# Performance work log

Hardware: AMD Instinct MI355X
Metric: run time of the kernel (lower is better)

## Reference

```python
import jax, jax.numpy as jnp
import numpy as np

E, C, D, H = 32, 4096, 256, 1024

def setup_inputs() -> dict:
    key = jax.random.key(0)
    kx, k1, k2 = jax.random.split(key, 3)
    x = jax.random.normal(kx, (E, C, D), dtype=jnp.float32)
    w1 = jax.random.normal(k1, (E, D, H), dtype=jnp.float32) * 0.02
    w2 = jax.random.normal(k2, (E, H, D), dtype=jnp.float32) * 0.02
    b1 = jnp.zeros((E, H), dtype=jnp.float32)
    b2 = jnp.zeros((E, D), dtype=jnp.float32)
    bungee = jnp.ones((E,), dtype=jnp.float32)  # bungee_init = 1.0, per-expert
    return {"x": x, "w1": w1, "b1": b1, "w2": w2, "b2": b2, "bungee": bungee}

def reference(x, w1, b1, w2, b2, bungee):
    # per-expert MLP: [E,C,D] @ [E,D,H] -> bias -> exact GELU -> [E,C,H] @ [E,H,D] -> bias -> scale
    h = jnp.einsum('ecd,edh->ech', x, w1) + b1[:, None, :]
    h = jax.nn.gelu(h, approximate=False)
    y = jnp.einsum('ech,ehd->ecd', h, w2) + b2[:, None, :]
    y = y * bungee[:, None, None]
    expert_out_rms = jnp.sqrt(jnp.mean(jnp.square(y)))
    bungee_mean = jnp.mean(bungee)
    bungee_min = jnp.min(bungee)
    bungee_max = jnp.max(bungee)
    return (y, expert_out_rms, bungee_mean, bungee_min, bungee_max)
```

## Files before the change

### kernel.cpp

```cpp
#include <hip/hip_runtime.h>
#include <cmath>

#define NE 32
#define NC 4096
#define ND 256
#define NH 1024
#define BM 64
#define BH 128
#define NSTEP (NH / BH)
#define NWAVE 8
#define THREADS (NWAVE * 64)
#define NWG (NE * NC / BM)
#define TOTY ((size_t)NE * NC * ND)

typedef float  float4v __attribute__((ext_vector_type(4)));
typedef float  f32x4   __attribute__((ext_vector_type(4)));
typedef short  short8v __attribute__((ext_vector_type(8)));
typedef short  short4v __attribute__((ext_vector_type(4)));
typedef __bf16 bf16x8  __attribute__((ext_vector_type(8)));
typedef __bf16 bf16x4  __attribute__((ext_vector_type(4)));

__device__ inline unsigned short f2bf(float f) {
  unsigned int u = __float_as_uint(f);
  u += 0x7fffu + ((u >> 16) & 1u);
  return (unsigned short)(u >> 16);
}

__device__ inline f32x4 mfma16(bf16x8 a, bf16x8 b, f32x4 c) {
  return __builtin_amdgcn_mfma_f32_16x16x32_bf16(a, b, c, 0, 0, 0);
}

__device__ inline float gelu_fast(float v) {
  float u = v * 0.70710678118f;
  float a = fabsf(u);
  float t = __builtin_amdgcn_rcpf(__builtin_fmaf(0.3275911f, a, 1.0f));
  float p = 1.061405429f;
  p = __builtin_fmaf(p, t, -1.453152027f);
  p = __builtin_fmaf(p, t, 1.421413741f);
  p = __builtin_fmaf(p, t, -0.284496736f);
  p = __builtin_fmaf(p, t, 0.254829592f);
  p = p * t;
  float e = __expf(-u * u);
  float erf_a = 1.0f - p * e;
  float erf_u = copysignf(erf_a, u);
  return 0.5f * v * (1.0f + erf_u);
}

__device__ inline float gelu_exact(float v) {
  return 0.5f * v * (1.0f + erff(v * 0.70710678118f));
}

__global__ void transpose_cvt(const float* __restrict__ src, unsigned short* __restrict__ dst,
                              int R, int Cc) {
  __shared__ alignas(16) float tile[32][33];
  int tilesC = Cc >> 5;
  int per_e  = (R >> 5) * tilesC;
  int e  = blockIdx.x / per_e;
  int t  = blockIdx.x % per_e;
  int tr = t / tilesC, tc = t % tilesC;
  const float* s = src + (size_t)e * R * Cc;
  unsigned short* d = dst + (size_t)e * R * Cc;
  int tx = threadIdx.x & 31, ty = threadIdx.x >> 5;
  for (int i = ty; i < 32; i += 8)
    tile[i][tx] = s[(size_t)(tr * 32 + i) * Cc + tc * 32 + tx];
  __syncthreads();
  for (int i = ty; i < 32; i += 8)
    d[(size_t)(tc * 32 + i) * R + tr * 32 + tx] = f2bf(tile[tx][i]);
}

__global__ void zero_scalar(float* p) {
  if (threadIdx.x == 0 && blockIdx.x == 0) *p = 0.0f;
}

__global__ __launch_bounds__(THREADS, 4) void experts_mlp(
    const float* __restrict__ x, const float* __restrict__ b1,
    const float* __restrict__ b2, const float* __restrict__ bungee,
    const unsigned short* __restrict__ w1t, const unsigned short* __restrict__ w2t,
    float* __restrict__ y, float* __restrict__ sumsq) {
  __shared__ alignas(16) unsigned char x_sw[BM * 512];
  __shared__ alignas(16) short h_lds[BM][BH + 8];
  __shared__ float red[NWAVE];

  int bid = blockIdx.x;
  int wg  = (bid & 7) * (NWG / 8) + (bid >> 3);
  int e   = wg >> 6;
  int r0  = (wg & 63) * BM;

  int tid  = threadIdx.x;
  int wid  = tid >> 6;
  int lane = tid & 63;
  int lr   = lane & 15;
  int lg   = lane >> 4;
  int lr7  = lr & 7;

  {
    const float* xb = x + ((size_t)e * NC + r0) * ND;
    #pragma unroll
    for (int j = 0; j < 8; ++j) {
      int f   = j * 512 + tid;
      int row = f >> 6;
      int c16 = f & 63;
      float4v u = *(const float4v*)(xb + (size_t)f * 4);
      bf16x4 s;
      s[0] = (__bf16)u[0]; s[1] = (__bf16)u[1]; s[2] = (__bf16)u[2]; s[3] = (__bf16)u[3];
      int cb = c16 * 8;
      *(bf16x4*)(x_sw + row * 512 + (cb ^ ((row & 7) << 6))) = s;
    }
  }
  __syncthreads();

  f32x4 zero4 = {0.f, 0.f, 0.f, 0.f};
  f32x4 acc2[2][4];
  #pragma unroll
  for (int mf = 0; mf < 2; ++mf)
    #pragma unroll
    for (int nf = 0; nf < 4; ++nf) acc2[mf][nf] = zero4;

  const unsigned short* w1row = w1t + ((size_t)e * NH + wid * 16 + lr) * ND;
  const unsigned short* w2row = w2t + ((size_t)e * ND + wid * 32 + lr) * NH;

  for (int hs = 0; hs < NSTEP; ++hs) {
    bf16x8 a1[8];
    const unsigned short* wr = w1row + (size_t)hs * BH * ND;
    #pragma unroll
    for (int ks = 0; ks < 8; ++ks)
      a1[ks] = __builtin_bit_cast(bf16x8, *(const short8v*)(wr + ks * 32 + lg * 8));

    f32x4 acc1[4];
    #pragma unroll
    for (int nf = 0; nf < 4; ++nf) acc1[nf] = zero4;
    #pragma unroll
    for (int ks = 0; ks < 8; ++ks) {
      int kx = (ks ^ lr7) * 64 + lg * 16;
      #pragma unroll
      for (int nf = 0; nf < 4; ++nf) {
        int row = nf * 16 + lr;
        bf16x8 xv = *(const bf16x8*)(x_sw + row * 512 + kx);
        acc1[nf] = mfma16(a1[ks], xv, acc1[nf]);
      }
    }

    int clocal = wid * 16 + lg * 4;
    const float* b1p = b1 + (size_t)e * NH + hs * BH + clocal;
    float4v bv = *(const float4v*)b1p;
    #pragma unroll
    for (int nf = 0; nf < 4; ++nf) {
      bf16x4 p;
      #pragma unroll
      for (int reg = 0; reg < 4; ++reg)
        p[reg] = (__bf16)gelu_fast(acc1[nf][reg] + bv[reg]);
      *(bf16x4*)&h_lds[nf * 16 + lr][clocal] = p;
    }
    __syncthreads();

    const unsigned short* w2p = w2row + (size_t)hs * BH;
    #pragma unroll
    for (int ks = 0; ks < 4; ++ks) {
      bf16x8 a20 = __builtin_bit_cast(bf16x8, *(const short8v*)(w2p + ks * 32 + lg * 8));
      bf16x8 a21 = __builtin_bit_cast(bf16x8, *(const short8v*)(w2p + (size_t)16 * NH + ks * 32 + lg * 8));
      #pragma unroll
      for (int nf = 0; nf < 4; ++nf) {
        bf16x8 hb = __builtin_bit_cast(bf16x8, *(const short8v*)&h_lds[nf * 16 + lr][ks * 32 + lg * 8]);
        acc2[0][nf] = mfma16(a20, hb, acc2[0][nf]);
        acc2[1][nf] = mfma16(a21, hb, acc2[1][nf]);
      }
    }
    __syncthreads();
  }

  float bg = bungee[e];
  float ss = 0.0f;
  int dbase = wid * 32 + lg * 4;
  #pragma unroll
  for (int mf = 0; mf < 2; ++mf) {
    int dd = dbase + mf * 16;
    float4v b2v = *(const float4v*)(b2 + (size_t)e * ND + dd);
    #pragma unroll
    for (int nf = 0; nf < 4; ++nf) {
      int r = r0 + nf * 16 + lr;
      float4v o;
      #pragma unroll
      for (int reg = 0; reg < 4; ++reg) {
        float v = (acc2[mf][nf][reg] + b2v[reg]) * bg;
        o[reg] = v;
        ss += v * v;
      }
      *(float4v*)(y + ((size_t)e * NC + r) * ND + dd) = o;
    }
  }
  #pragma unroll
  for (int off = 32; off > 0; off >>= 1) ss += __shfl_down(ss, off);
  if (lane == 0) red[wid] = ss;
  __syncthreads();
  if (tid == 0) {
    float t = 0.f;
    #pragma unroll
    for (int i = 0; i < NWAVE; ++i) t += red[i];
    atomicAdd(sumsq, t);
  }
}

#define FBROWS 8
__global__ __launch_bounds__(256) void fb_mlp(
    const float* __restrict__ x, const float* __restrict__ w1, const float* __restrict__ b1,
    const float* __restrict__ w2, const float* __restrict__ b2, const float* __restrict__ bungee,
    float* __restrict__ y, float* __restrict__ sumsq) {
  __shared__ alignas(16) float xs[FBROWS][ND];
  __shared__ alignas(16) float hsh[FBROWS][NH];
  __shared__ float red[4];
  int tid = threadIdx.x;
  int e  = blockIdx.x / (NC / FBROWS);
  int r0 = (blockIdx.x % (NC / FBROWS)) * FBROWS;

  for (int i = tid; i < FBROWS * ND; i += 256)
    ((float*)xs)[i] = x[((size_t)e * NC + r0) * ND + i];
  __syncthreads();

  for (int c = tid; c < NH; c += 256) {
    float acc[FBROWS];
    float bb = b1[(size_t)e * NH + c];
    #pragma unroll
    for (int rr = 0; rr < FBROWS; ++rr) acc[rr] = bb;
    for (int k = 0; k < ND; ++k) {
      float w = w1[((size_t)e * ND + k) * NH + c];
      #pragma unroll
      for (int rr = 0; rr < FBROWS; ++rr) acc[rr] += xs[rr][k] * w;
    }
    #pragma unroll
    for (int rr = 0; rr < FBROWS; ++rr) hsh[rr][c] = gelu_exact(acc[rr]);
  }
  __syncthreads();

  int d = tid;
  float acc[FBROWS];
  float bb = b2[(size_t)e * ND + d];
  #pragma unroll
  for (int rr = 0; rr < FBROWS; ++rr) acc[rr] = bb;
  for (int c = 0; c < NH; ++c) {
    float w = w2[((size_t)e * NH + c) * ND + d];
    #pragma unroll
    for (int rr = 0; rr < FBROWS; ++rr) acc[rr] += hsh[rr][c] * w;
  }
  float bg = bungee[e];
  float ss = 0.f;
  #pragma unroll
  for (int rr = 0; rr < FBROWS; ++rr) {
    float v = acc[rr] * bg;
    y[((size_t)e * NC + r0 + rr) * ND + d] = v;
    ss += v * v;
  }
  #pragma unroll
  for (int off = 32; off > 0; off >>= 1) ss += __shfl_down(ss, off);
  if ((tid & 63) == 0) red[tid >> 6] = ss;
  __syncthreads();
  if (tid == 0) atomicAdd(sumsq, red[0] + red[1] + red[2] + red[3]);
}

__global__ void finalize(const float* __restrict__ bungee, float* __restrict__ out_scalars) {
  if (threadIdx.x == 0 && blockIdx.x == 0) {
    float ss = out_scalars[0];
    out_scalars[0] = sqrtf(ss / (float)TOTY);
    float m = 0.f, mn = bungee[0], mx = bungee[0];
    for (int i = 0; i < NE; ++i) {
      float b = bungee[i];
      m += b; mn = fminf(mn, b); mx = fmaxf(mx, b);
    }
    out_scalars[1] = m / (float)NE;
    out_scalars[2] = mn;
    out_scalars[3] = mx;
  }
}

extern "C" void kernel_launch(void* const* d_in, const int* in_sizes, int n_in,
                              void* d_out, int out_size, void* d_ws, size_t ws_size,
                              hipStream_t stream) {
  (void)in_sizes; (void)n_in; (void)out_size;
  const float* x  = (const float*)d_in[0];
  const float* w1 = (const float*)d_in[1];
  const float* b1 = (const float*)d_in[2];
  const float* w2 = (const float*)d_in[3];
  const float* b2 = (const float*)d_in[4];
  const float* bg = (const float*)d_in[5];
  float* out = (float*)d_out;
  float* rms_slot = out + TOTY;

  const size_t WS_NEEDED = (size_t)NE * ND * NH * 2 * 2;

  zero_scalar<<<1, 1, 0, stream>>>(rms_slot);
  if (ws_size >= WS_NEEDED) {
    unsigned short* w1t = (unsigned short*)d_ws;
    unsigned short* w2t = w1t + (size_t)NE * ND * NH;
    transpose_cvt<<<NE * (ND / 32) * (NH / 32), 256, 0, stream>>>(w1, w1t, ND, NH);
    transpose_cvt<<<NE * (NH / 32) * (ND / 32), 256, 0, stream>>>(w2, w2t, NH, ND);
    experts_mlp<<<NWG, THREADS, 0, stream>>>(x, b1, b2, bg, w1t, w2t, out, rms_slot);
  } else {
    fb_mlp<<<NE * NC / FBROWS, 256, 0, stream>>>(x, w1, b1, w2, b2, bg, out, rms_slot);
  }
  finalize<<<1, 64, 0, stream>>>(bg, rms_slot);
}
```

Measured before the change: 547.2 us.

## Prefetch next-step W1 fragments and hoist W2 loads; fuse prep kernels

Software-pipelines the weight fragment loads in the expert MLP loop. W2 fragments are issued at the top of each step and the next step's W1 fragments are loaded after the first GEMM, so global latency overlaps with MFMA work. The first W1 load moves ahead of the initial barrier. The two transpose kernels and the zeroing kernel are merged into one prep launch to cut launch overhead. The added in-flight fragments raise register pressure, which may reduce occupancy under the 4-waves launch bound.

```diff
diff --git a/kernel.cpp b/kernel.cpp
--- a/kernel.cpp
+++ b/kernel.cpp
@@ -50,13 +50,19 @@
   return 0.5f * v * (1.0f + erff(v * 0.70710678118f));
 }
 
-__global__ void transpose_cvt(const float* __restrict__ src, unsigned short* __restrict__ dst,
-                              int R, int Cc) {
+__global__ void prep(const float* __restrict__ w1, const float* __restrict__ w2,
+                     unsigned short* __restrict__ w1t, unsigned short* __restrict__ w2t,
+                     float* __restrict__ rms_slot) {
+  if (blockIdx.x == 0 && threadIdx.x == 0) *rms_slot = 0.0f;
   __shared__ alignas(16) float tile[32][33];
+  int b = blockIdx.x;
+  const float* src; unsigned short* dst; int R, Cc;
+  if (b < 8192) { src = w1; dst = w1t; R = ND; Cc = NH; }
+  else          { b -= 8192; src = w2; dst = w2t; R = NH; Cc = ND; }
   int tilesC = Cc >> 5;
   int per_e  = (R >> 5) * tilesC;
-  int e  = blockIdx.x / per_e;
-  int t  = blockIdx.x % per_e;
+  int e  = b / per_e;
+  int t  = b % per_e;
   int tr = t / tilesC, tc = t % tilesC;
   const float* s = src + (size_t)e * R * Cc;
   unsigned short* d = dst + (size_t)e * R * Cc;
@@ -107,7 +113,6 @@
       *(bf16x4*)(x_sw + row * 512 + (cb ^ ((row & 7) << 6))) = s;
     }
   }
-  __syncthreads();
 
   f32x4 zero4 = {0.f, 0.f, 0.f, 0.f};
   f32x4 acc2[2][4];
@@ -119,12 +124,21 @@
   const unsigned short* w1row = w1t + ((size_t)e * NH + wid * 16 + lr) * ND;
   const unsigned short* w2row = w2t + ((size_t)e * ND + wid * 32 + lr) * NH;
 
+  bf16x8 a1[8];
+  #pragma unroll
+  for (int ks = 0; ks < 8; ++ks)
+    a1[ks] = __builtin_bit_cast(bf16x8, *(const short8v*)(w1row + ks * 32 + lg * 8));
+
+  __syncthreads();
+
   for (int hs = 0; hs < NSTEP; ++hs) {
-    bf16x8 a1[8];
-    const unsigned short* wr = w1row + (size_t)hs * BH * ND;
-    #pragma unroll
-    for (int ks = 0; ks < 8; ++ks)
-      a1[ks] = __builtin_bit_cast(bf16x8, *(const short8v*)(wr + ks * 32 + lg * 8));
+    const unsigned short* w2p = w2row + (size_t)hs * BH;
+    bf16x8 w2f0[4], w2f1[4];
+    #pragma unroll
+    for (int ks = 0; ks < 4; ++ks) {
+      w2f0[ks] = __builtin_bit_cast(bf16x8, *(const short8v*)(w2p + ks * 32 + lg * 8));
+      w2f1[ks] = __builtin_bit_cast(bf16x8, *(const short8v*)(w2p + (size_t)16 * NH + ks * 32 + lg * 8));
+    }
 
     f32x4 acc1[4];
     #pragma unroll
@@ -140,6 +154,13 @@
       }
     }
 
+    if (hs + 1 < NSTEP) {
+      const unsigned short* wr = w1row + (size_t)(hs + 1) * BH * ND;
+      #pragma unroll
+      for (int ks = 0; ks < 8; ++ks)
+        a1[ks] = __builtin_bit_cast(bf16x8, *(const short8v*)(wr + ks * 32 + lg * 8));
+    }
+
     int clocal = wid * 16 + lg * 4;
     const float* b1p = b1 + (size_t)e * NH + hs * BH + clocal;
     float4v bv = *(const float4v*)b1p;
@@ -153,16 +174,13 @@
     }
     __syncthreads();
 
-    const unsigned short* w2p = w2row + (size_t)hs * BH;
     #pragma unroll
     for (int ks = 0; ks < 4; ++ks) {
-      bf16x8 a20 = __builtin_bit_cast(bf16x8, *(const short8v*)(w2p + ks * 32 + lg * 8));
-      bf16x8 a21 = __builtin_bit_cast(bf16x8, *(const short8v*)(w2p + (size_t)16 * NH + ks * 32 + lg * 8));
       #pragma unroll
       for (int nf = 0; nf < 4; ++nf) {
         bf16x8 hb = __builtin_bit_cast(bf16x8, *(const short8v*)&h_lds[nf * 16 + lr][ks * 32 + lg * 8]);
-        acc2[0][nf] = mfma16(a20, hb, acc2[0][nf]);
-        acc2[1][nf] = mfma16(a21, hb, acc2[1][nf]);
+        acc2[0][nf] = mfma16(w2f0[ks], hb, acc2[0][nf]);
+        acc2[1][nf] = mfma16(w2f1[ks], hb, acc2[1][nf]);
       }
     }
     __syncthreads();
@@ -286,14 +304,13 @@
 
   const size_t WS_NEEDED = (size_t)NE * ND * NH * 2 * 2;
 
-  zero_scalar<<<1, 1, 0, stream>>>(rms_slot);
   if (ws_size >= WS_NEEDED) {
     unsigned short* w1t = (unsigned short*)d_ws;
     unsigned short* w2t = w1t + (size_t)NE * ND * NH;
-    transpose_cvt<<<NE * (ND / 32) * (NH / 32), 256, 0, stream>>>(w1, w1t, ND, NH);
-    transpose_cvt<<<NE * (NH / 32) * (ND / 32), 256, 0, stream>>>(w2, w2t, NH, ND);
+    prep<<<16384, 256, 0, stream>>>(w1, w2, w1t, w2t, rms_slot);
     experts_mlp<<<NWG, THREADS, 0, stream>>>(x, b1, b2, bg, w1t, w2t, out, rms_slot);
   } else {
+    zero_scalar<<<1, 1, 0, stream>>>(rms_slot);
     fb_mlp<<<NE * NC / FBROWS, 256, 0, stream>>>(x, w1, b1, w2, b2, bg, out, rms_slot);
   }
   finalize<<<1, 64, 0, stream>>>(bg, rms_slot);
```

Measured after the change: 520.8 us. 4.8% less time.
